# Optimization experiments

Hardware: AMD Instinct MI355X
Metric: run time of the kernel (lower is better)

## Reference

```python
import jax, jax.numpy as jnp
from jax import lax
import numpy as np

B, INP, WIDTH, OUTP, E, H = 32, 1024, 256, 1024, 8, 14
EPS = 1e-5


def setup_inputs() -> dict:
    key = jax.random.key(0)
    ks = jax.random.split(key, 12)
    n = lambda k, s, sc=0.05: jax.random.normal(k, s, jnp.float32) * sc
    return {
        "x": jax.random.normal(ks[0], (B, INP, H, H), jnp.float32),
        "w1": n(ks[1], (E, WIDTH, INP, 1, 1)),
        "w2": n(ks[2], (E, WIDTH, WIDTH, 3, 3)),
        "w3": n(ks[3], (E, OUTP, WIDTH, 1, 1)),
        "r1_w": n(ks[4], (INP, E)), "r1_b": jnp.zeros((E,), jnp.float32),
        "r2_w": n(ks[5], (WIDTH, E)), "r2_b": jnp.zeros((E,), jnp.float32),
        "r3_w": n(ks[6], (WIDTH, E)), "r3_b": jnp.zeros((E,), jnp.float32),
        "bn1_g": jax.random.uniform(ks[7], (WIDTH,), jnp.float32, 0.5, 1.5),
        "bn1_b": n(ks[8], (WIDTH,), 0.1),
        "bn1_m": jnp.zeros((WIDTH,), jnp.float32), "bn1_v": jnp.ones((WIDTH,), jnp.float32),
        "bn2_g": jax.random.uniform(ks[9], (WIDTH,), jnp.float32, 0.5, 1.5),
        "bn2_b": n(ks[10], (WIDTH,), 0.1),
        "bn2_m": jnp.zeros((WIDTH,), jnp.float32), "bn2_v": jnp.ones((WIDTH,), jnp.float32),
        "bn3_g": jax.random.uniform(ks[11], (OUTP,), jnp.float32, 0.5, 1.5),
        "bn3_b": jnp.zeros((OUTP,), jnp.float32),
        "bn3_m": jnp.zeros((OUTP,), jnp.float32), "bn3_v": jnp.ones((OUTP,), jnp.float32),
    }


def _route(x, w, b):
    # global avg pool -> linear -> sigmoid : [B, E]
    return jax.nn.sigmoid(x.mean(axis=(2, 3)) @ w + b)


def _cond_conv(x, w, rw, stride=1, padding=0, dilation=1, groups=1):
    # x: [B,Cin,H,W]; w: [E,Cout,Cin/groups,kh,kw]; rw: [B,E]
    Bn, Cin, Hh, Ww = x.shape
    _, Cout, Cin_g, kh, kw = w.shape
    # per-sample expert-combined kernels, then batch-grouped conv
    cw = jnp.einsum('be,eoikl->boikl', rw, w).reshape(Bn * Cout, Cin_g, kh, kw)
    out = lax.conv_general_dilated(
        x.reshape(1, Bn * Cin, Hh, Ww), cw,
        window_strides=(stride, stride),
        padding=[(padding, padding), (padding, padding)],
        rhs_dilation=(dilation, dilation),
        feature_group_count=Bn * groups,
        dimension_numbers=('NCHW', 'OIHW', 'NCHW'))
    return out.reshape(Bn, Cout, out.shape[2], out.shape[3])


def _bn(x, g, b, m, v):
    inv = lax.rsqrt(v + EPS) * g
    return x * inv[None, :, None, None] + (b - m * inv)[None, :, None, None]


def reference(x, w1, w2, w3, r1_w, r1_b, r2_w, r2_b, r3_w, r3_b,
              bn1_g, bn1_b, bn1_m, bn1_v, bn2_g, bn2_b, bn2_m, bn2_v,
              bn3_g, bn3_b, bn3_m, bn3_v):
    identity = x
    rw1 = _route(x, r1_w, r1_b)
    out = jax.nn.relu(_bn(_cond_conv(x, w1, rw1), bn1_g, bn1_b, bn1_m, bn1_v))
    rw2 = _route(out, r2_w, r2_b)
    out = jax.nn.relu(_bn(_cond_conv(out, w2, rw2, stride=1, padding=1), bn2_g, bn2_b, bn2_m, bn2_v))
    rw3 = _route(out, r3_w, r3_b)
    out = _bn(_cond_conv(out, w3, rw3), bn3_g, bn3_b, bn3_m, bn3_v)
    return jax.nn.relu(out + identity)
```

## Files before the change

kernel.cpp:

```cpp
#include <hip/hip_runtime.h>
#include <hip/hip_bf16.h>

#define BB 32
#define INP 1024
#define WIDTH 256
#define OUTP 1024
#define NE 8
#define HW 196
#define HH 14
#define EPS 1e-5f

#define S1 (WIDTH * INP)
#define S2 (WIDTH * WIDTH * 9)
#define S3 (OUTP * WIDTH)

typedef __attribute__((ext_vector_type(8))) short bf16x8;
typedef __attribute__((ext_vector_type(4))) float f32x4;
typedef __attribute__((ext_vector_type(8))) unsigned short u16x8;


__device__ __forceinline__ unsigned short f2bf_bits(float f) {
    unsigned u = __float_as_uint(f);
    u += 0x7FFFu + ((u >> 16) & 1u);
    return (unsigned short)(u >> 16);
}

#if defined(__has_builtin)
#if __has_builtin(__builtin_amdgcn_global_load_lds)
#define HAVE_GLL 1
#endif
#endif
__device__ __forceinline__ void gl2lds(const unsigned short* g, unsigned short* l,
                                       int lane) {
#ifdef HAVE_GLL
    __builtin_amdgcn_global_load_lds(
        (const __attribute__((address_space(1))) unsigned int*)(const void*)g,
        (__attribute__((address_space(3))) unsigned int*)(void*)l, 16, 0, 0);
#else
    *(u16x8*)(l + lane * 8) = *(const u16x8*)g;
#endif
}

__device__ __forceinline__ void block_route(
    const float* __restrict__ vec, const float* __restrict__ W,
    const float* __restrict__ bias, float scale, int C, int g,
    float* srw, int tid) {
    int wv = tid >> 6, lane = tid & 63;
    float p0[NE], p1[NE];
#pragma unroll
    for (int e = 0; e < NE; e++) { p0[e] = 0.f; p1[e] = 0.f; }
    const float* v0 = vec + (size_t)(g * 8 + wv * 2) * C;
    const float* v1 = v0 + C;
    for (int c = lane; c < C; c += 64) {
        float4 wa = *(const float4*)(W + c * 8);
        float4 wb = *(const float4*)(W + c * 8 + 4);
        float m0 = v0[c], m1 = v1[c];
        p0[0] += m0 * wa.x; p0[1] += m0 * wa.y; p0[2] += m0 * wa.z; p0[3] += m0 * wa.w;
        p0[4] += m0 * wb.x; p0[5] += m0 * wb.y; p0[6] += m0 * wb.z; p0[7] += m0 * wb.w;
        p1[0] += m1 * wa.x; p1[1] += m1 * wa.y; p1[2] += m1 * wa.z; p1[3] += m1 * wa.w;
        p1[4] += m1 * wb.x; p1[5] += m1 * wb.y; p1[6] += m1 * wb.z; p1[7] += m1 * wb.w;
    }
#pragma unroll
    for (int j = 1; j < 64; j <<= 1) {
#pragma unroll
        for (int e = 0; e < NE; e++) {
            p0[e] += __shfl_xor(p0[e], j, 64);
            p1[e] += __shfl_xor(p1[e], j, 64);
        }
    }
    if (lane == 0) {
#pragma unroll
        for (int e = 0; e < NE; e++) {
            srw[(wv * 2) * 8 + e] = 1.0f / (1.0f + expf(-(scale * p0[e] + bias[e])));
            srw[(wv * 2 + 1) * 8 + e] = 1.0f / (1.0f + expf(-(scale * p1[e] + bias[e])));
        }
    }
    __syncthreads();
}

__global__ __launch_bounds__(256) void transpose_mean_x(
    const float* __restrict__ x, unsigned short* __restrict__ xb,
    float* __restrict__ mean1) {
    __shared__ float lt[128][17];
    int b = blockIdx.x, c0 = blockIdx.y * 128;
    int t = threadIdx.x, cr = t >> 1, half = t & 1;
    const float* src = x + ((size_t)(b * INP + c0 + cr)) * HW;
    float msum = 0.f;
    int j = t >> 4, nl = t & 15;
    for (int pg = 0; pg < 14; pg++) {
        int p0 = pg * 16 + half * 8;
        float vv[8];
        if (pg < 12) {
            float4 a = *(const float4*)(src + p0);
            float4 c = *(const float4*)(src + p0 + 4);
            vv[0] = a.x; vv[1] = a.y; vv[2] = a.z; vv[3] = a.w;
            vv[4] = c.x; vv[5] = c.y; vv[6] = c.z; vv[7] = c.w;
        } else {
#pragma unroll
            for (int i = 0; i < 8; i++) {
                int p = p0 + i;
                vv[i] = (p < HW) ? src[p] : 0.f;
            }
        }
#pragma unroll
        for (int i = 0; i < 8; i++) { msum += vv[i]; lt[cr][half * 8 + i] = vv[i]; }
        __syncthreads();
        unsigned short pk[8];
#pragma unroll
        for (int i = 0; i < 8; i++) pk[i] = f2bf_bits(lt[j * 8 + i][nl]);
        size_t tile = ((size_t)b * 14 + pg) * 32 + (size_t)(blockIdx.y * 4 + (j >> 2));
        int lane = nl | ((j & 3) << 4);
        *(u16x8*)(xb + tile * 512 + lane * 8) = *(u16x8*)pk;
        __syncthreads();
    }
    float other = __shfl_xor(msum, 1, 64);
    if (half == 0) mean1[b * INP + c0 + cr] = (msum + other) * (1.0f / (float)HW);
}

__global__ __launch_bounds__(256) void combine_cont_r(
    const float* __restrict__ w, const float* __restrict__ vec,
    const float* __restrict__ rW, const float* __restrict__ rB, float scale, int C,
    unsigned short* __restrict__ cw, int S, int Mt, int Kt) {
    __shared__ float srw[64];
    int tid = threadIdx.x, wv = tid >> 6, lane = tid & 63, ml = lane & 15, k8l = lane >> 4;
    int g = blockIdx.y;
    block_route(vec, rW, rB, scale, C, g, srw, tid);
    int kq = Kt >> 2;
    int mt = blockIdx.x / kq, kt = (blockIdx.x - mt * kq) * 4 + wv;
    int K = Kt * 32;
    const float* src = w + (size_t)(mt * 16 + ml) * K + kt * 32 + k8l * 8;
    float v[NE][8];
#pragma unroll
    for (int e = 0; e < NE; e++) {
        float4 a = *(const float4*)(src + (size_t)e * S);
        float4 c = *(const float4*)(src + (size_t)e * S + 4);
        v[e][0] = a.x; v[e][1] = a.y; v[e][2] = a.z; v[e][3] = a.w;
        v[e][4] = c.x; v[e][5] = c.y; v[e][6] = c.z; v[e][7] = c.w;
    }
    size_t dto = ((size_t)mt * Kt + kt) * 512 + (size_t)lane * 8;
    size_t bstr = (size_t)Mt * Kt * 512;
    for (int bl = 0; bl < 8; bl++) {
        int b = g * 8 + bl;
        float acc[8];
#pragma unroll
        for (int jj = 0; jj < 8; jj++) acc[jj] = 0.f;
#pragma unroll
        for (int e = 0; e < NE; e++) {
            float r = srw[bl * NE + e];
#pragma unroll
            for (int jj = 0; jj < 8; jj++) acc[jj] += r * v[e][jj];
        }
        u16x8 o;
#pragma unroll
        for (int jj = 0; jj < 8; jj++) o[jj] = f2bf_bits(acc[jj]);
        *(u16x8*)(cw + (size_t)b * bstr + dto) = o;
    }
}

__global__ __launch_bounds__(256) void permute_w2(
    const float* __restrict__ w2, unsigned short* __restrict__ wb2) {
    __shared__ unsigned short lds[9 * 256];
    int eo = blockIdx.x, t = threadIdx.x;
    const float* src = w2 + (size_t)eo * 2304 + (size_t)t * 9;
#pragma unroll
    for (int t9 = 0; t9 < 9; t9++) lds[t9 * 256 + t] = f2bf_bits(src[t9]);
    __syncthreads();
    unsigned short* dst = wb2 + (size_t)eo * 2304;
    for (int j = t; j < 288; j += 256)
        *(u16x8*)(dst + j * 8) = *(const u16x8*)(lds + j * 8);
}

__global__ __launch_bounds__(256) void combine_w2_r(
    const unsigned short* __restrict__ wb2, const float* __restrict__ vec,
    const float* __restrict__ rW, const float* __restrict__ rB, float scale,
    unsigned short* __restrict__ cw) {
    __shared__ float srw[64];
    int tid = threadIdx.x, wv = tid >> 6, lane = tid & 63, ol = lane & 15, g4 = lane >> 4;
    int g = blockIdx.y;
    block_route(vec, rW, rB, scale, 256, g, srw, tid);
    int ot = blockIdx.x / 18, kt = (blockIdx.x - ot * 18) * 4 + wv;
    const unsigned short* src = wb2 + (size_t)(ot * 16 + ol) * 2304 + kt * 32 + g4 * 8;
    float v[NE][8];
#pragma unroll
    for (int e = 0; e < NE; e++) {
        u16x8 raw = *(const u16x8*)(src + (size_t)e * S2);
#pragma unroll
        for (int jj = 0; jj < 8; jj++)
            v[e][jj] = __uint_as_float((unsigned)raw[jj] << 16);
    }
    size_t dto = ((size_t)ot * 72 + kt) * 512 + (size_t)lane * 8;
    for (int bl = 0; bl < 8; bl++) {
        int b = g * 8 + bl;
        float acc[8];
#pragma unroll
        for (int jj = 0; jj < 8; jj++) acc[jj] = 0.f;
#pragma unroll
        for (int e = 0; e < NE; e++) {
            float r = srw[bl * NE + e];
#pragma unroll
            for (int jj = 0; jj < 8; jj++) acc[jj] += r * v[e][jj];
        }
        u16x8 out;
#pragma unroll
        for (int jj = 0; jj < 8; jj++) out[jj] = f2bf_bits(acc[jj]);
        *(u16x8*)(cw + (size_t)b * (16 * 72 * 512) + dto) = out;
    }
}

__device__ __forceinline__ void epilogue_act(
    const f32x4* acc, int b, int mt, int nh, int lo, int g4,
    const float* __restrict__ g, const float* __restrict__ be,
    const float* __restrict__ mu, const float* __restrict__ var,
    unsigned short* __restrict__ actout, float* __restrict__ msum) {
    int c0 = mt * 16 + g4 * 4;
    float sc[4], sh[4];
#pragma unroll
    for (int r = 0; r < 4; r++) {
        float iv = rsqrtf(var[c0 + r] + EPS) * g[c0 + r];
        sc[r] = iv;
        sh[r] = be[c0 + r] - mu[c0 + r] * iv;
    }
    float ms[4] = {0.f, 0.f, 0.f, 0.f};
    int ktc = mt >> 1;
    int lanehi = ((mt * 2 + (g4 >> 1)) & 3) << 4;
#pragma unroll
    for (int t = 0; t < 7; t++) {
        int nt = nh * 7 + t;
        int n = nt * 16 + lo;
        float v[4];
#pragma unroll
        for (int r = 0; r < 4; r++) {
            float val = acc[t][r] * sc[r] + sh[r];
            val = fmaxf(val, 0.f);
            if (n >= HW) val = 0.f;
            v[r] = val;
            ms[r] += val;
        }
        unsigned p01 = (unsigned)f2bf_bits(v[0]) | ((unsigned)f2bf_bits(v[1]) << 16);
        unsigned p23 = (unsigned)f2bf_bits(v[2]) | ((unsigned)f2bf_bits(v[3]) << 16);
        size_t off = (((size_t)(b * 14 + nt)) * 8 + ktc) * 512 + (size_t)(lo | lanehi) * 8 + (g4 & 1) * 4;
        *(uint2*)(actout + off) = make_uint2(p01, p23);
    }
#pragma unroll
    for (int r = 0; r < 4; r++) {
        float s = ms[r];
        s += __shfl_xor(s, 1, 64);
        s += __shfl_xor(s, 2, 64);
        s += __shfl_xor(s, 4, 64);
        s += __shfl_xor(s, 8, 64);
        if (lo == 0) atomicAdd(&msum[b * 256 + c0 + r], s);
    }
}

__global__ __launch_bounds__(256) void gemm1_fused(
    const unsigned short* __restrict__ Bsw, const unsigned short* __restrict__ Asw,
    const float* __restrict__ g, const float* __restrict__ be,
    const float* __restrict__ mu, const float* __restrict__ var,
    unsigned short* __restrict__ actout, float* __restrict__ msum) {
    __shared__ __align__(16) unsigned short lAb[4][4 * 512];
    __shared__ __align__(16) unsigned short lBb[4][7 * 512];
    const int Kt = 32;
    int b = blockIdx.x, mh = blockIdx.y, nh = blockIdx.z;
    int tid = threadIdx.x, wv = tid >> 6, lane = tid & 63, lo = lane & 15, g4 = lane >> 4;
    const unsigned short* Ab = Asw + (size_t)(b * 16 + mh * 4) * Kt * 512;
    const unsigned short* Bb = Bsw + (size_t)(b * 14 + nh * 7) * Kt * 512;
    f32x4 acc[7];
#pragma unroll
    for (int t = 0; t < 7; t++) acc[t] = {0.f, 0.f, 0.f, 0.f};

    auto stage = [&](int kt, unsigned short* lA, unsigned short* lB) {
        gl2lds(Ab + ((size_t)wv * Kt + kt) * 512 + lane * 8, lA + wv * 512, lane);
        gl2lds(Bb + ((size_t)wv * Kt + kt) * 512 + lane * 8, lB + wv * 512, lane);
        if (wv < 3)
            gl2lds(Bb + ((size_t)(4 + wv) * Kt + kt) * 512 + lane * 8, lB + (4 + wv) * 512, lane);
    };
    auto compute = [&](const unsigned short* lA, const unsigned short* lB) {
        bf16x8 a0 = *(const bf16x8*)(lA + wv * 512 + lane * 8);
#pragma unroll
        for (int t = 0; t < 7; t++) {
            bf16x8 bt = *(const bf16x8*)(lB + t * 512 + lane * 8);
            acc[t] = __builtin_amdgcn_mfma_f32_16x16x32_bf16(a0, bt, acc[t], 0, 0, 0);
        }
    };

    stage(0, lAb[0], lBb[0]);
    stage(1, lAb[1], lBb[1]);
    for (int kp = 0; kp < 16; kp++) {
        int cb = (kp & 1) << 1, sb = 2 - cb;
        __syncthreads();
        if (kp < 15) {
            stage(2 * kp + 2, lAb[sb], lBb[sb]);
            stage(2 * kp + 3, lAb[sb + 1], lBb[sb + 1]);
        }
        compute(lAb[cb], lBb[cb]);
        compute(lAb[cb + 1], lBb[cb + 1]);
    }
    epilogue_act(acc, b, mh * 4 + wv, nh, lo, g4, g, be, mu, var, actout, msum);
}

__global__ __launch_bounds__(256) void gemm2_fused(
    const unsigned short* __restrict__ act, const unsigned short* __restrict__ cw2,
    const unsigned short* __restrict__ zpad,
    const float* __restrict__ g, const float* __restrict__ be,
    const float* __restrict__ mu, const float* __restrict__ var,
    unsigned short* __restrict__ actout, float* __restrict__ msum) {
    __shared__ __align__(16) unsigned short lAb[4][4 * 512];
    __shared__ __align__(16) unsigned short lBb[4][7 * 512];
    int b = blockIdx.x, mh = blockIdx.y, nh = blockIdx.z;
    int tid = threadIdx.x, wv = tid >> 6, lane = tid & 63, lo = lane & 15, g4 = lane >> 4;
    const unsigned short* Ab = cw2 + (size_t)(b * 16 + mh * 4) * 72 * 512;
    const unsigned short* actb = act + (size_t)b * 14 * 8 * 512;

    int p0 = (nh * 7 + wv) * 16 + lo;
    int py0 = p0 / HH, px0 = p0 - (p0 / HH) * HH;
    bool pv0 = p0 < HW;
    int p1 = (nh * 7 + wv + 4) * 16 + lo;
    int py1 = p1 / HH, px1 = p1 - (p1 / HH) * HH;
    bool pv1 = (wv < 3) && (p1 < HW);

    f32x4 acc[7];
#pragma unroll
    for (int t = 0; t < 7; t++) acc[t] = {0.f, 0.f, 0.f, 0.f};

    auto stage = [&](int kt, unsigned short* lA, unsigned short* lB) {
        gl2lds(Ab + ((size_t)wv * 72 + kt) * 512 + lane * 8, lA + wv * 512, lane);
        int t9 = kt >> 3;
        int dy = t9 / 3 - 1, dx = t9 - (t9 / 3) * 3 - 1;
        int itile = kt & 7;
        {
            int sy = py0 + dy, sx = px0 + dx;
            bool ok = pv0 && sy >= 0 && sy < HH && sx >= 0 && sx < HH;
            int ns = sy * HH + sx;
            const unsigned short* gp = ok
                ? actb + ((size_t)(ns >> 4) * 8 + itile) * 512 + (size_t)((ns & 15) | (g4 << 4)) * 8
                : zpad;
            gl2lds(gp, lB + wv * 512, lane);
        }
        if (wv < 3) {
            int sy = py1 + dy, sx = px1 + dx;
            bool ok = pv1 && sy >= 0 && sy < HH && sx >= 0 && sx < HH;
            int ns = sy * HH + sx;
            const unsigned short* gp = ok
                ? actb + ((size_t)(ns >> 4) * 8 + itile) * 512 + (size_t)((ns & 15) | (g4 << 4)) * 8
                : zpad;
            gl2lds(gp, lB + (wv + 4) * 512, lane);
        }
    };
    auto compute = [&](const unsigned short* lA, const unsigned short* lB) {
        bf16x8 a0 = *(const bf16x8*)(lA + wv * 512 + lane * 8);
#pragma unroll
        for (int t = 0; t < 7; t++) {
            bf16x8 bt = *(const bf16x8*)(lB + t * 512 + lane * 8);
            acc[t] = __builtin_amdgcn_mfma_f32_16x16x32_bf16(a0, bt, acc[t], 0, 0, 0);
        }
    };

    stage(0, lAb[0], lBb[0]);
    stage(1, lAb[1], lBb[1]);
    for (int kp = 0; kp < 36; kp++) {
        int cb = (kp & 1) << 1, sb = 2 - cb;
        __syncthreads();
        if (kp < 35) {
            stage(2 * kp + 2, lAb[sb], lBb[sb]);
            stage(2 * kp + 3, lAb[sb + 1], lBb[sb + 1]);
        }
        compute(lAb[cb], lBb[cb]);
        compute(lAb[cb + 1], lBb[cb + 1]);
    }
    epilogue_act(acc, b, mh * 4 + wv, nh, lo, g4, g, be, mu, var, actout, msum);
}

__global__ __launch_bounds__(256) void gemm3_fused(
    const unsigned short* __restrict__ Bsw, const unsigned short* __restrict__ Asw,
    const float* __restrict__ g, const float* __restrict__ be,
    const float* __restrict__ mu, const float* __restrict__ var,
    const float* __restrict__ resid, float* __restrict__ out) {
    __shared__ __align__(16) unsigned short lAb[4][8 * 512];
    __shared__ __align__(16) unsigned short lBb[4][7 * 512];
    int b = blockIdx.x, y = blockIdx.y, mh = y >> 1, nh = y & 1;
    int tid = threadIdx.x, wv = tid >> 6, lane = tid & 63, lo = lane & 15, g4 = lane >> 4;
    const unsigned short* Ab = Asw + (size_t)(b * 64 + mh * 8) * 8 * 512;
    const unsigned short* Bb = Bsw + (size_t)(b * 14 + nh * 7) * 8 * 512;
    f32x4 acc0[7], acc1[7];
#pragma unroll
    for (int t = 0; t < 7; t++) { acc0[t] = {0.f, 0.f, 0.f, 0.f}; acc1[t] = {0.f, 0.f, 0.f, 0.f}; }

    auto stage = [&](int kt, unsigned short* lA, unsigned short* lB) {
        gl2lds(Ab + ((size_t)wv * 8 + kt) * 512 + lane * 8, lA + wv * 512, lane);
        gl2lds(Ab + ((size_t)(wv + 4) * 8 + kt) * 512 + lane * 8, lA + (wv + 4) * 512, lane);
        gl2lds(Bb + ((size_t)wv * 8 + kt) * 512 + lane * 8, lB + wv * 512, lane);
        if (wv < 3)
            gl2lds(Bb + ((size_t)(4 + wv) * 8 + kt) * 512 + lane * 8, lB + (4 + wv) * 512, lane);
    };
    auto compute = [&](const unsigned short* lA, const unsigned short* lB) {
        bf16x8 a0 = *(const bf16x8*)(lA + wv * 512 + lane * 8);
        bf16x8 a1 = *(const bf16x8*)(lA + (wv + 4) * 512 + lane * 8);
#pragma unroll
        for (int t = 0; t < 7; t++) {
            bf16x8 bt = *(const bf16x8*)(lB + t * 512 + lane * 8);
            acc0[t] = __builtin_amdgcn_mfma_f32_16x16x32_bf16(a0, bt, acc0[t], 0, 0, 0);
            acc1[t] = __builtin_amdgcn_mfma_f32_16x16x32_bf16(a1, bt, acc1[t], 0, 0, 0);
        }
    };

    stage(0, lAb[0], lBb[0]);
    stage(1, lAb[1], lBb[1]);
#pragma unroll
    for (int kp = 0; kp < 4; kp++) {
        int cb = (kp & 1) << 1, sb = 2 - cb;
        __syncthreads();
        if (kp + 1 < 4) {
            stage(2 * kp + 2, lAb[sb], lBb[sb]);
            stage(2 * kp + 3, lAb[sb + 1], lBb[sb + 1]);
        }
        compute(lAb[cb], lBb[cb]);
        compute(lAb[cb + 1], lBb[cb + 1]);
    }
#pragma unroll
    for (int a = 0; a < 2; a++) {
        int mt = mh * 8 + wv + 4 * a;
        int c0 = mt * 16 + g4 * 4;
        float sc[4], sh[4];
#pragma unroll
        for (int r = 0; r < 4; r++) {
            float iv = rsqrtf(var[c0 + r] + EPS) * g[c0 + r];
            sc[r] = iv;
            sh[r] = be[c0 + r] - mu[c0 + r] * iv;
        }
#pragma unroll
        for (int t = 0; t < 7; t++) {
            int n = (nh * 7 + t) * 16 + lo;
            if (n >= HW) continue;
            f32x4 av = a ? acc1[t] : acc0[t];
#pragma unroll
            for (int r = 0; r < 4; r++) {
                size_t oidx = ((size_t)(b * OUTP + c0 + r)) * HW + n;
                float val = av[r] * sc[r] + sh[r] + resid[oidx];
                out[oidx] = fmaxf(val, 0.f);
            }
        }
    }
}

extern "C" void kernel_launch(void* const* d_in, const int* in_sizes, int n_in,
                              void* d_out, int out_size, void* d_ws, size_t ws_size,
                              hipStream_t stream) {
    const float* x    = (const float*)d_in[0];
    const float* w1   = (const float*)d_in[1];
    const float* w2   = (const float*)d_in[2];
    const float* w3   = (const float*)d_in[3];
    const float* r1_w = (const float*)d_in[4];
    const float* r1_b = (const float*)d_in[5];
    const float* r2_w = (const float*)d_in[6];
    const float* r2_b = (const float*)d_in[7];
    const float* r3_w = (const float*)d_in[8];
    const float* r3_b = (const float*)d_in[9];
    const float* bn1_g = (const float*)d_in[10];
    const float* bn1_b = (const float*)d_in[11];
    const float* bn1_m = (const float*)d_in[12];
    const float* bn1_v = (const float*)d_in[13];
    const float* bn2_g = (const float*)d_in[14];
    const float* bn2_b = (const float*)d_in[15];
    const float* bn2_m = (const float*)d_in[16];
    const float* bn2_v = (const float*)d_in[17];
    const float* bn3_g = (const float*)d_in[18];
    const float* bn3_b = (const float*)d_in[19];
    const float* bn3_m = (const float*)d_in[20];
    const float* bn3_v = (const float*)d_in[21];
    float* out = (float*)d_out;

    char* ws = (char*)d_ws;
    size_t off = 0;
    float* mean1 = (float*)(ws + off); off += (size_t)BB * INP * 4;
    float* msum2 = (float*)(ws + off); off += (size_t)BB * 256 * 4;
    float* msum3 = (float*)(ws + off); off += (size_t)BB * 256 * 4;
    unsigned short* zpad = (unsigned short*)(ws + off); off += 256;
    off = (off + 255) & ~(size_t)255;
    unsigned short* act1 = (unsigned short*)(ws + off); off += (size_t)BB * 14 * 8 * 512 * 2;
    unsigned short* act2 = (unsigned short*)(ws + off); off += (size_t)BB * 14 * 8 * 512 * 2;
    unsigned short* cw2 = (unsigned short*)(ws + off); off += (size_t)BB * 16 * 72 * 512 * 2;
    char* regionA = ws + off; off += (size_t)BB * (14 + 16) * 32 * 512 * 2;
    unsigned short* xb  = (unsigned short*)regionA;
    unsigned short* cw1 = (unsigned short*)(regionA + (size_t)BB * 14 * 32 * 512 * 2);
    unsigned short* wb2 = (unsigned short*)regionA;
    unsigned short* cw3 = (unsigned short*)regionA;
    (void)ws_size;

    hipMemsetAsync(msum2, 0, (size_t)2 * BB * 256 * 4 + 256, stream);
    transpose_mean_x<<<dim3(BB, 8), 256, 0, stream>>>(x, xb, mean1);

    combine_cont_r<<<dim3(128, 4), 256, 0, stream>>>(w1, mean1, r1_w, r1_b, 1.0f, INP,
                                                     cw1, S1, 16, 32);
    gemm1_fused<<<dim3(BB, 4, 2), 256, 0, stream>>>(xb, cw1, bn1_g, bn1_b, bn1_m, bn1_v,
                                                    act1, msum2);
    permute_w2<<<2048, 256, 0, stream>>>(w2, wb2);

    combine_w2_r<<<dim3(288, 4), 256, 0, stream>>>(wb2, msum2, r2_w, r2_b,
                                                   1.0f / (float)HW, cw2);
    gemm2_fused<<<dim3(BB, 4, 2), 256, 0, stream>>>(act1, cw2, zpad, bn2_g, bn2_b,
                                                    bn2_m, bn2_v, act2, msum3);

    combine_cont_r<<<dim3(128, 4), 256, 0, stream>>>(w3, msum3, r3_w, r3_b,
                                                     1.0f / (float)HW, WIDTH,
                                                     cw3, S3, 64, 8);
    gemm3_fused<<<dim3(BB, 16), 256, 0, stream>>>(act2, cw3, bn3_g, bn3_b, bn3_m, bn3_v,
                                                  x, out);
}
```

Baseline: 254.6 us.

## Split-K GEMMs over two wave groups, fuse w2 permute, bf16 residual

All three GEMM kernels now run 512 threads as two 4-wave groups. Each group handles alternate K tiles through a 4-slot LDS ring, and the partial accumulators are reduced through LDS before the epilogue. The aim is more waves per block to hide load latency on a grid that is small relative to the CU count. The w2 permute is folded into the x-transpose kernel as extra blocks, which saves one launch. The final residual add now reads the bf16 transposed copy of x instead of fp32 x, which cuts memory traffic but adds bf16 rounding error to the identity path. Workspace buffers are no longer aliased so that xb survives until the last kernel.

```diff
diff --git a/kernel.cpp b/kernel.cpp
--- a/kernel.cpp
+++ b/kernel.cpp
@@ -23,6 +23,9 @@
     unsigned u = __float_as_uint(f);
     u += 0x7FFFu + ((u >> 16) & 1u);
     return (unsigned short)(u >> 16);
+}
+__device__ __forceinline__ float bf2f(unsigned short h) {
+    return __uint_as_float((unsigned)h << 16);
 }
 
 #if defined(__has_builtin)
@@ -78,43 +81,58 @@
     __syncthreads();
 }
 
-__global__ __launch_bounds__(256) void transpose_mean_x(
+__global__ __launch_bounds__(256) void pre_kernel(
     const float* __restrict__ x, unsigned short* __restrict__ xb,
-    float* __restrict__ mean1) {
-    __shared__ float lt[128][17];
-    int b = blockIdx.x, c0 = blockIdx.y * 128;
-    int t = threadIdx.x, cr = t >> 1, half = t & 1;
-    const float* src = x + ((size_t)(b * INP + c0 + cr)) * HW;
-    float msum = 0.f;
-    int j = t >> 4, nl = t & 15;
-    for (int pg = 0; pg < 14; pg++) {
-        int p0 = pg * 16 + half * 8;
-        float vv[8];
-        if (pg < 12) {
-            float4 a = *(const float4*)(src + p0);
-            float4 c = *(const float4*)(src + p0 + 4);
-            vv[0] = a.x; vv[1] = a.y; vv[2] = a.z; vv[3] = a.w;
-            vv[4] = c.x; vv[5] = c.y; vv[6] = c.z; vv[7] = c.w;
-        } else {
-#pragma unroll
-            for (int i = 0; i < 8; i++) {
-                int p = p0 + i;
-                vv[i] = (p < HW) ? src[p] : 0.f;
+    float* __restrict__ mean1,
+    const float* __restrict__ w2, unsigned short* __restrict__ wb2) {
+    __shared__ __align__(16) char smem[128 * 17 * 4];
+    int blk = blockIdx.x, t = threadIdx.x;
+    if (blk < 256) {
+        float (*lt)[17] = (float(*)[17])smem;
+        int b = blk >> 3, yq = blk & 7, c0 = yq * 128;
+        int cr = t >> 1, half = t & 1;
+        const float* src = x + ((size_t)(b * INP + c0 + cr)) * HW;
+        float msum = 0.f;
+        int j = t >> 4, nl = t & 15;
+        for (int pg = 0; pg < 14; pg++) {
+            int p0 = pg * 16 + half * 8;
+            float vv[8];
+            if (pg < 12) {
+                float4 a = *(const float4*)(src + p0);
+                float4 c = *(const float4*)(src + p0 + 4);
+                vv[0] = a.x; vv[1] = a.y; vv[2] = a.z; vv[3] = a.w;
+                vv[4] = c.x; vv[5] = c.y; vv[6] = c.z; vv[7] = c.w;
+            } else {
+#pragma unroll
+                for (int i = 0; i < 8; i++) {
+                    int p = p0 + i;
+                    vv[i] = (p < HW) ? src[p] : 0.f;
+                }
             }
-        }
-#pragma unroll
-        for (int i = 0; i < 8; i++) { msum += vv[i]; lt[cr][half * 8 + i] = vv[i]; }
+#pragma unroll
+            for (int i = 0; i < 8; i++) { msum += vv[i]; lt[cr][half * 8 + i] = vv[i]; }
+            __syncthreads();
+            unsigned short pk[8];
+#pragma unroll
+            for (int i = 0; i < 8; i++) pk[i] = f2bf_bits(lt[j * 8 + i][nl]);
+            size_t tile = ((size_t)b * 14 + pg) * 32 + (size_t)(yq * 4 + (j >> 2));
+            int lane = nl | ((j & 3) << 4);
+            *(u16x8*)(xb + tile * 512 + lane * 8) = *(u16x8*)pk;
+            __syncthreads();
+        }
+        float other = __shfl_xor(msum, 1, 64);
+        if (half == 0) mean1[b * INP + c0 + cr] = (msum + other) * (1.0f / (float)HW);
+    } else {
+        unsigned short* lds = (unsigned short*)smem;
+        int eo = blk - 256;
+        const float* src = w2 + (size_t)eo * 2304 + (size_t)t * 9;
+#pragma unroll
+        for (int t9 = 0; t9 < 9; t9++) lds[t9 * 256 + t] = f2bf_bits(src[t9]);
         __syncthreads();
-        unsigned short pk[8];
-#pragma unroll
-        for (int i = 0; i < 8; i++) pk[i] = f2bf_bits(lt[j * 8 + i][nl]);
-        size_t tile = ((size_t)b * 14 + pg) * 32 + (size_t)(blockIdx.y * 4 + (j >> 2));
-        int lane = nl | ((j & 3) << 4);
-        *(u16x8*)(xb + tile * 512 + lane * 8) = *(u16x8*)pk;
-        __syncthreads();
-    }
-    float other = __shfl_xor(msum, 1, 64);
-    if (half == 0) mean1[b * INP + c0 + cr] = (msum + other) * (1.0f / (float)HW);
+        unsigned short* dst = wb2 + (size_t)eo * 2304;
+        for (int j = t; j < 288; j += 256)
+            *(u16x8*)(dst + j * 8) = *(const u16x8*)(lds + j * 8);
+    }
 }
 
 __global__ __launch_bounds__(256) void combine_cont_r(
@@ -157,19 +175,6 @@
     }
 }
 
-__global__ __launch_bounds__(256) void permute_w2(
-    const float* __restrict__ w2, unsigned short* __restrict__ wb2) {
-    __shared__ unsigned short lds[9 * 256];
-    int eo = blockIdx.x, t = threadIdx.x;
-    const float* src = w2 + (size_t)eo * 2304 + (size_t)t * 9;
-#pragma unroll
-    for (int t9 = 0; t9 < 9; t9++) lds[t9 * 256 + t] = f2bf_bits(src[t9]);
-    __syncthreads();
-    unsigned short* dst = wb2 + (size_t)eo * 2304;
-    for (int j = t; j < 288; j += 256)
-        *(u16x8*)(dst + j * 8) = *(const u16x8*)(lds + j * 8);
-}
-
 __global__ __launch_bounds__(256) void combine_w2_r(
     const unsigned short* __restrict__ wb2, const float* __restrict__ vec,
     const float* __restrict__ rW, const float* __restrict__ rB, float scale,
@@ -185,8 +190,7 @@
     for (int e = 0; e < NE; e++) {
         u16x8 raw = *(const u16x8*)(src + (size_t)e * S2);
 #pragma unroll
-        for (int jj = 0; jj < 8; jj++)
-            v[e][jj] = __uint_as_float((unsigned)raw[jj] << 16);
+        for (int jj = 0; jj < 8; jj++) v[e][jj] = bf2f(raw[jj]);
     }
     size_t dto = ((size_t)ot * 72 + kt) * 512 + (size_t)lane * 8;
     for (int bl = 0; bl < 8; bl++) {
@@ -252,7 +256,7 @@
     }
 }
 
-__global__ __launch_bounds__(256) void gemm1_fused(
+__global__ __launch_bounds__(512) void gemm1_fused(
     const unsigned short* __restrict__ Bsw, const unsigned short* __restrict__ Asw,
     const float* __restrict__ g, const float* __restrict__ be,
     const float* __restrict__ mu, const float* __restrict__ var,
@@ -261,7 +265,8 @@
     __shared__ __align__(16) unsigned short lBb[4][7 * 512];
     const int Kt = 32;
     int b = blockIdx.x, mh = blockIdx.y, nh = blockIdx.z;
-    int tid = threadIdx.x, wv = tid >> 6, lane = tid & 63, lo = lane & 15, g4 = lane >> 4;
+    int tid = threadIdx.x, wv = tid >> 6, grp = wv >> 2, wl = wv & 3;
+    int lane = tid & 63, lo = lane & 15, g4 = lane >> 4;
     const unsigned short* Ab = Asw + (size_t)(b * 16 + mh * 4) * Kt * 512;
     const unsigned short* Bb = Bsw + (size_t)(b * 14 + nh * 7) * Kt * 512;
     f32x4 acc[7];
@@ -269,13 +274,13 @@
     for (int t = 0; t < 7; t++) acc[t] = {0.f, 0.f, 0.f, 0.f};
 
     auto stage = [&](int kt, unsigned short* lA, unsigned short* lB) {
-        gl2lds(Ab + ((size_t)wv * Kt + kt) * 512 + lane * 8, lA + wv * 512, lane);
-        gl2lds(Bb + ((size_t)wv * Kt + kt) * 512 + lane * 8, lB + wv * 512, lane);
-        if (wv < 3)
-            gl2lds(Bb + ((size_t)(4 + wv) * Kt + kt) * 512 + lane * 8, lB + (4 + wv) * 512, lane);
+        gl2lds(Ab + ((size_t)wl * Kt + kt) * 512 + lane * 8, lA + wl * 512, lane);
+        gl2lds(Bb + ((size_t)wl * Kt + kt) * 512 + lane * 8, lB + wl * 512, lane);
+        if (wl < 3)
+            gl2lds(Bb + ((size_t)(4 + wl) * Kt + kt) * 512 + lane * 8, lB + (4 + wl) * 512, lane);
     };
     auto compute = [&](const unsigned short* lA, const unsigned short* lB) {
-        bf16x8 a0 = *(const bf16x8*)(lA + wv * 512 + lane * 8);
+        bf16x8 a0 = *(const bf16x8*)(lA + wl * 512 + lane * 8);
 #pragma unroll
         for (int t = 0; t < 7; t++) {
             bf16x8 bt = *(const bf16x8*)(lB + t * 512 + lane * 8);
@@ -283,22 +288,36 @@
         }
     };
 
-    stage(0, lAb[0], lBb[0]);
-    stage(1, lAb[1], lBb[1]);
+    stage(grp, lAb[grp], lBb[grp]);
     for (int kp = 0; kp < 16; kp++) {
-        int cb = (kp & 1) << 1, sb = 2 - cb;
         __syncthreads();
         if (kp < 15) {
-            stage(2 * kp + 2, lAb[sb], lBb[sb]);
-            stage(2 * kp + 3, lAb[sb + 1], lBb[sb + 1]);
-        }
-        compute(lAb[cb], lBb[cb]);
-        compute(lAb[cb + 1], lBb[cb + 1]);
-    }
-    epilogue_act(acc, b, mh * 4 + wv, nh, lo, g4, g, be, mu, var, actout, msum);
-}
-
-__global__ __launch_bounds__(256) void gemm2_fused(
+            int s = 2 * kp + 2 + grp;
+            stage(s, lAb[s & 3], lBb[s & 3]);
+        }
+        int c = (2 * kp + grp) & 3;
+        compute(lAb[c], lBb[c]);
+    }
+    __syncthreads();
+    float* red = (float*)&lBb[0][0];
+    if (grp == 1) {
+#pragma unroll
+        for (int t = 0; t < 7; t++)
+            *(f32x4*)(red + (((size_t)wl * 7 + t) * 64 + lane) * 4) = acc[t];
+    }
+    __syncthreads();
+    if (grp == 0) {
+#pragma unroll
+        for (int t = 0; t < 7; t++) {
+            f32x4 o = *(const f32x4*)(red + (((size_t)wl * 7 + t) * 64 + lane) * 4);
+#pragma unroll
+            for (int r = 0; r < 4; r++) acc[t][r] += o[r];
+        }
+        epilogue_act(acc, b, mh * 4 + wl, nh, lo, g4, g, be, mu, var, actout, msum);
+    }
+}
+
+__global__ __launch_bounds__(512) void gemm2_fused(
     const unsigned short* __restrict__ act, const unsigned short* __restrict__ cw2,
     const unsigned short* __restrict__ zpad,
     const float* __restrict__ g, const float* __restrict__ be,
@@ -307,23 +326,24 @@
     __shared__ __align__(16) unsigned short lAb[4][4 * 512];
     __shared__ __align__(16) unsigned short lBb[4][7 * 512];
     int b = blockIdx.x, mh = blockIdx.y, nh = blockIdx.z;
-    int tid = threadIdx.x, wv = tid >> 6, lane = tid & 63, lo = lane & 15, g4 = lane >> 4;
+    int tid = threadIdx.x, wv = tid >> 6, grp = wv >> 2, wl = wv & 3;
+    int lane = tid & 63, lo = lane & 15, g4 = lane >> 4;
     const unsigned short* Ab = cw2 + (size_t)(b * 16 + mh * 4) * 72 * 512;
     const unsigned short* actb = act + (size_t)b * 14 * 8 * 512;
 
-    int p0 = (nh * 7 + wv) * 16 + lo;
+    int p0 = (nh * 7 + wl) * 16 + lo;
     int py0 = p0 / HH, px0 = p0 - (p0 / HH) * HH;
     bool pv0 = p0 < HW;
-    int p1 = (nh * 7 + wv + 4) * 16 + lo;
+    int p1 = (nh * 7 + wl + 4) * 16 + lo;
     int py1 = p1 / HH, px1 = p1 - (p1 / HH) * HH;
-    bool pv1 = (wv < 3) && (p1 < HW);
+    bool pv1 = (wl < 3) && (p1 < HW);
 
     f32x4 acc[7];
 #pragma unroll
     for (int t = 0; t < 7; t++) acc[t] = {0.f, 0.f, 0.f, 0.f};
 
     auto stage = [&](int kt, unsigned short* lA, unsigned short* lB) {
-        gl2lds(Ab + ((size_t)wv * 72 + kt) * 512 + lane * 8, lA + wv * 512, lane);
+        gl2lds(Ab + ((size_t)wl * 72 + kt) * 512 + lane * 8, lA + wl * 512, lane);
         int t9 = kt >> 3;
         int dy = t9 / 3 - 1, dx = t9 - (t9 / 3) * 3 - 1;
         int itile = kt & 7;
@@ -334,20 +354,20 @@
             const unsigned short* gp = ok
                 ? actb + ((size_t)(ns >> 4) * 8 + itile) * 512 + (size_t)((ns & 15) | (g4 << 4)) * 8
                 : zpad;
-            gl2lds(gp, lB + wv * 512, lane);
-        }
-        if (wv < 3) {
+            gl2lds(gp, lB + wl * 512, lane);
+        }
+        if (wl < 3) {
             int sy = py1 + dy, sx = px1 + dx;
             bool ok = pv1 && sy >= 0 && sy < HH && sx >= 0 && sx < HH;
             int ns = sy * HH + sx;
             const unsigned short* gp = ok
                 ? actb + ((size_t)(ns >> 4) * 8 + itile) * 512 + (size_t)((ns & 15) | (g4 << 4)) * 8
                 : zpad;
-            gl2lds(gp, lB + (wv + 4) * 512, lane);
+            gl2lds(gp, lB + (wl + 4) * 512, lane);
         }
     };
     auto compute = [&](const unsigned short* lA, const unsigned short* lB) {
-        bf16x8 a0 = *(const bf16x8*)(lA + wv * 512 + lane * 8);
+        bf16x8 a0 = *(const bf16x8*)(lA + wl * 512 + lane * 8);
 #pragma unroll
         for (int t = 0; t < 7; t++) {
             bf16x8 bt = *(const bf16x8*)(lB + t * 512 + lane * 8);
@@ -355,30 +375,45 @@
         }
     };
 
-    stage(0, lAb[0], lBb[0]);
-    stage(1, lAb[1], lBb[1]);
+    stage(grp, lAb[grp], lBb[grp]);
     for (int kp = 0; kp < 36; kp++) {
-        int cb = (kp & 1) << 1, sb = 2 - cb;
         __syncthreads();
         if (kp < 35) {
-            stage(2 * kp + 2, lAb[sb], lBb[sb]);
-            stage(2 * kp + 3, lAb[sb + 1], lBb[sb + 1]);
-        }
-        compute(lAb[cb], lBb[cb]);
-        compute(lAb[cb + 1], lBb[cb + 1]);
-    }
-    epilogue_act(acc, b, mh * 4 + wv, nh, lo, g4, g, be, mu, var, actout, msum);
-}
-
-__global__ __launch_bounds__(256) void gemm3_fused(
+            int s = 2 * kp + 2 + grp;
+            stage(s, lAb[s & 3], lBb[s & 3]);
+        }
+        int c = (2 * kp + grp) & 3;
+        compute(lAb[c], lBb[c]);
+    }
+    __syncthreads();
+    float* red = (float*)&lBb[0][0];
+    if (grp == 1) {
+#pragma unroll
+        for (int t = 0; t < 7; t++)
+            *(f32x4*)(red + (((size_t)wl * 7 + t) * 64 + lane) * 4) = acc[t];
+    }
+    __syncthreads();
+    if (grp == 0) {
+#pragma unroll
+        for (int t = 0; t < 7; t++) {
+            f32x4 o = *(const f32x4*)(red + (((size_t)wl * 7 + t) * 64 + lane) * 4);
+#pragma unroll
+            for (int r = 0; r < 4; r++) acc[t][r] += o[r];
+        }
+        epilogue_act(acc, b, mh * 4 + wl, nh, lo, g4, g, be, mu, var, actout, msum);
+    }
+}
+
+__global__ __launch_bounds__(512) void gemm3_fused(
     const unsigned short* __restrict__ Bsw, const unsigned short* __restrict__ Asw,
     const float* __restrict__ g, const float* __restrict__ be,
     const float* __restrict__ mu, const float* __restrict__ var,
-    const float* __restrict__ resid, float* __restrict__ out) {
+    const unsigned short* __restrict__ xb, float* __restrict__ out) {
     __shared__ __align__(16) unsigned short lAb[4][8 * 512];
     __shared__ __align__(16) unsigned short lBb[4][7 * 512];
     int b = blockIdx.x, y = blockIdx.y, mh = y >> 1, nh = y & 1;
-    int tid = threadIdx.x, wv = tid >> 6, lane = tid & 63, lo = lane & 15, g4 = lane >> 4;
+    int tid = threadIdx.x, wv = tid >> 6, grp = wv >> 2, wl = wv & 3;
+    int lane = tid & 63, lo = lane & 15, g4 = lane >> 4;
     const unsigned short* Ab = Asw + (size_t)(b * 64 + mh * 8) * 8 * 512;
     const unsigned short* Bb = Bsw + (size_t)(b * 14 + nh * 7) * 8 * 512;
     f32x4 acc0[7], acc1[7];
@@ -386,15 +421,15 @@
     for (int t = 0; t < 7; t++) { acc0[t] = {0.f, 0.f, 0.f, 0.f}; acc1[t] = {0.f, 0.f, 0.f, 0.f}; }
 
     auto stage = [&](int kt, unsigned short* lA, unsigned short* lB) {
-        gl2lds(Ab + ((size_t)wv * 8 + kt) * 512 + lane * 8, lA + wv * 512, lane);
-        gl2lds(Ab + ((size_t)(wv + 4) * 8 + kt) * 512 + lane * 8, lA + (wv + 4) * 512, lane);
-        gl2lds(Bb + ((size_t)wv * 8 + kt) * 512 + lane * 8, lB + wv * 512, lane);
-        if (wv < 3)
-            gl2lds(Bb + ((size_t)(4 + wv) * 8 + kt) * 512 + lane * 8, lB + (4 + wv) * 512, lane);
+        gl2lds(Ab + ((size_t)wl * 8 + kt) * 512 + lane * 8, lA + wl * 512, lane);
+        gl2lds(Ab + ((size_t)(wl + 4) * 8 + kt) * 512 + lane * 8, lA + (wl + 4) * 512, lane);
+        gl2lds(Bb + ((size_t)wl * 8 + kt) * 512 + lane * 8, lB + wl * 512, lane);
+        if (wl < 3)
+            gl2lds(Bb + ((size_t)(4 + wl) * 8 + kt) * 512 + lane * 8, lB + (4 + wl) * 512, lane);
     };
     auto compute = [&](const unsigned short* lA, const unsigned short* lB) {
-        bf16x8 a0 = *(const bf16x8*)(lA + wv * 512 + lane * 8);
-        bf16x8 a1 = *(const bf16x8*)(lA + (wv + 4) * 512 + lane * 8);
+        bf16x8 a0 = *(const bf16x8*)(lA + wl * 512 + lane * 8);
+        bf16x8 a1 = *(const bf16x8*)(lA + (wl + 4) * 512 + lane * 8);
 #pragma unroll
         for (int t = 0; t < 7; t++) {
             bf16x8 bt = *(const bf16x8*)(lB + t * 512 + lane * 8);
@@ -403,22 +438,50 @@
         }
     };
 
-    stage(0, lAb[0], lBb[0]);
-    stage(1, lAb[1], lBb[1]);
-#pragma unroll
+    stage(grp, lAb[grp], lBb[grp]);
     for (int kp = 0; kp < 4; kp++) {
-        int cb = (kp & 1) << 1, sb = 2 - cb;
         __syncthreads();
-        if (kp + 1 < 4) {
-            stage(2 * kp + 2, lAb[sb], lBb[sb]);
-            stage(2 * kp + 3, lAb[sb + 1], lBb[sb + 1]);
-        }
-        compute(lAb[cb], lBb[cb]);
-        compute(lAb[cb + 1], lBb[cb + 1]);
-    }
+        if (kp < 3) {
+            int s = 2 * kp + 2 + grp;
+            stage(s, lAb[s & 3], lBb[s & 3]);
+        }
+        int c = (2 * kp + grp) & 3;
+        compute(lAb[c], lBb[c]);
+    }
+    __syncthreads();
+    float* red = (float*)&lBb[0][0];
+    if (grp == 1) {
+#pragma unroll
+        for (int t = 0; t < 7; t++)
+            *(f32x4*)(red + (((size_t)wl * 7 + t) * 64 + lane) * 4) = acc0[t];
+    }
+    __syncthreads();
+    if (grp == 0) {
+#pragma unroll
+        for (int t = 0; t < 7; t++) {
+            f32x4 o = *(const f32x4*)(red + (((size_t)wl * 7 + t) * 64 + lane) * 4);
+#pragma unroll
+            for (int r = 0; r < 4; r++) acc0[t][r] += o[r];
+        }
+    }
+    __syncthreads();
+    if (grp == 1) {
+#pragma unroll
+        for (int t = 0; t < 7; t++)
+            *(f32x4*)(red + (((size_t)wl * 7 + t) * 64 + lane) * 4) = acc1[t];
+    }
+    __syncthreads();
+    if (grp != 0) return;
+#pragma unroll
+    for (int t = 0; t < 7; t++) {
+        f32x4 o = *(const f32x4*)(red + (((size_t)wl * 7 + t) * 64 + lane) * 4);
+#pragma unroll
+        for (int r = 0; r < 4; r++) acc1[t][r] += o[r];
+    }
+
 #pragma unroll
     for (int a = 0; a < 2; a++) {
-        int mt = mh * 8 + wv + 4 * a;
+        int mt = mh * 8 + wl + 4 * a;
         int c0 = mt * 16 + g4 * 4;
         float sc[4], sh[4];
 #pragma unroll
@@ -427,15 +490,25 @@
             sc[r] = iv;
             sh[r] = be[c0 + r] - mu[c0 + r] * iv;
         }
-#pragma unroll
-        for (int t = 0; t < 7; t++) {
-            int n = (nh * 7 + t) * 16 + lo;
+        int ktc = mt >> 1;
+        int lanehi = ((mt * 2 + (g4 >> 1)) & 3) << 4;
+#pragma unroll
+        for (int t = 0; t < 7; t++) {
+            int nt = nh * 7 + t;
+            int n = nt * 16 + lo;
             if (n >= HW) continue;
+            const unsigned short* xr = xb + (((size_t)(b * 14 + nt)) * 32 + ktc) * 512
+                                       + (size_t)(lo | lanehi) * 8 + (g4 & 1) * 4;
+            uint2 rv = *(const uint2*)xr;
+            float res[4] = {bf2f((unsigned short)(rv.x & 0xffff)),
+                            bf2f((unsigned short)(rv.x >> 16)),
+                            bf2f((unsigned short)(rv.y & 0xffff)),
+                            bf2f((unsigned short)(rv.y >> 16))};
             f32x4 av = a ? acc1[t] : acc0[t];
 #pragma unroll
             for (int r = 0; r < 4; r++) {
                 size_t oidx = ((size_t)(b * OUTP + c0 + r)) * HW + n;
-                float val = av[r] * sc[r] + sh[r] + resid[oidx];
+                float val = av[r] * sc[r] + sh[r] + res[r];
                 out[oidx] = fmaxf(val, 0.f);
             }
         }
@@ -479,30 +552,30 @@
     unsigned short* act1 = (unsigned short*)(ws + off); off += (size_t)BB * 14 * 8 * 512 * 2;
     unsigned short* act2 = (unsigned short*)(ws + off); off += (size_t)BB * 14 * 8 * 512 * 2;
     unsigned short* cw2 = (unsigned short*)(ws + off); off += (size_t)BB * 16 * 72 * 512 * 2;
-    char* regionA = ws + off; off += (size_t)BB * (14 + 16) * 32 * 512 * 2;
-    unsigned short* xb  = (unsigned short*)regionA;
-    unsigned short* cw1 = (unsigned short*)(regionA + (size_t)BB * 14 * 32 * 512 * 2);
-    unsigned short* wb2 = (unsigned short*)regionA;
-    unsigned short* cw3 = (unsigned short*)regionA;
+    unsigned short* xb  = (unsigned short*)(ws + off); off += (size_t)BB * 14 * 32 * 512 * 2;
+    unsigned short* wb2 = (unsigned short*)(ws + off); off += (size_t)S2 * NE * 2;
+    unsigned short* cwX = (unsigned short*)(ws + off); off += (size_t)BB * S1 * 2;
+    unsigned short* cw1 = cwX;
+    unsigned short* cw3 = cwX;
     (void)ws_size;
 
     hipMemsetAsync(msum2, 0, (size_t)2 * BB * 256 * 4 + 256, stream);
-    transpose_mean_x<<<dim3(BB, 8), 256, 0, stream>>>(x, xb, mean1);
+
+    pre_kernel<<<2304, 256, 0, stream>>>(x, xb, mean1, w2, wb2);
 
     combine_cont_r<<<dim3(128, 4), 256, 0, stream>>>(w1, mean1, r1_w, r1_b, 1.0f, INP,
                                                      cw1, S1, 16, 32);
-    gemm1_fused<<<dim3(BB, 4, 2), 256, 0, stream>>>(xb, cw1, bn1_g, bn1_b, bn1_m, bn1_v,
+    gemm1_fused<<<dim3(BB, 4, 2), 512, 0, stream>>>(xb, cw1, bn1_g, bn1_b, bn1_m, bn1_v,
                                                     act1, msum2);
-    permute_w2<<<2048, 256, 0, stream>>>(w2, wb2);
 
     combine_w2_r<<<dim3(288, 4), 256, 0, stream>>>(wb2, msum2, r2_w, r2_b,
                                                    1.0f / (float)HW, cw2);
-    gemm2_fused<<<dim3(BB, 4, 2), 256, 0, stream>>>(act1, cw2, zpad, bn2_g, bn2_b,
+    gemm2_fused<<<dim3(BB, 4, 2), 512, 0, stream>>>(act1, cw2, zpad, bn2_g, bn2_b,
                                                     bn2_m, bn2_v, act2, msum3);
 
     combine_cont_r<<<dim3(128, 4), 256, 0, stream>>>(w3, msum3, r3_w, r3_b,
                                                      1.0f / (float)HW, WIDTH,
                                                      cw3, S3, 64, 8);
-    gemm3_fused<<<dim3(BB, 16), 256, 0, stream>>>(act2, cw3, bn3_g, bn3_b, bn3_m, bn3_v,
-                                                  x, out);
-}
+    gemm3_fused<<<dim3(BB, 16), 512, 0, stream>>>(act2, cw3, bn3_g, bn3_b, bn3_m, bn3_v,
+                                                  xb, out);
+}
```

Result: faster. 242.2 us (-4.9%).
